# Kernel tuning notes

Hardware: AMD Instinct MI355X
Metric: run time of the kernel (lower is better)

Reference implementation:

```python
import jax, jax.numpy as jnp
import numpy as np

Hh, Ww, Cc = 8, 8, 16        # observation grid h, w, channels
N = Hh * Ww                  # 64 graph nodes (one per grid cell)
B = 4096                     # batch
HEADS, COUT = 4, 32          # GAT heads, per-head output dim (concat -> 128)
HID, ADIM = 128, 6           # hidden_dim, action_dim
GAT_OUT = N * HEADS * COUT   # 8192 flattened GAT output per sample
NEG = -9e15


def _grid_adj():
    # 4-connected grid graph with self loops (make_graph's static edge structure)
    A = np.zeros((N, N), np.int32)
    for r in range(Hh):
        for c in range(Ww):
            i = r * Ww + c
            A[i, i] = 1
            for dr, dc in ((1, 0), (-1, 0), (0, 1), (0, -1)):
                rr, cc = r + dr, c + dc
                if 0 <= rr < Hh and 0 <= cc < Ww:
                    A[i, rr * Ww + cc] = 1
    return jnp.asarray(A)


def setup_inputs() -> dict:
    key = jax.random.key(0)
    ks = iter(jax.random.split(key, 40))
    p = lambda *s: jax.random.normal(next(ks), s, jnp.float32) * 0.1
    z = lambda *s: jnp.zeros(s, jnp.float32)
    return dict(
        x=jax.random.normal(next(ks), (B, Hh * Ww * Cc), jnp.float32),
        adj=_grid_adj(),
        actor_h=z(B, HID), actor_c=z(B, HID),
        critic_h=z(B, HID), critic_c=z(B, HID),
        gat1_W=p(Cc, HEADS * COUT), gat1_b=z(HEADS * COUT), gat1_a=p(HEADS, 2 * COUT),
        d1_W=p(GAT_OUT, HID), d1_b=z(HID),
        lstm1_Wi=p(HID, 4 * HID), lstm1_Wh=p(HID, 4 * HID), lstm1_b=z(4 * HID),
        ln1_s=jnp.ones((HID,), jnp.float32), ln1_bi=z(HID),
        d2_W=p(HID, HID), d2_b=z(HID),
        d3_W=p(HID, HID), d3_b=z(HID),
        dout_W=p(HID, ADIM), dout_b=z(ADIM),
        gat2_W=p(Cc, HEADS * COUT), gat2_b=z(HEADS * COUT), gat2_a=p(HEADS, 2 * COUT),
        c1_W=p(GAT_OUT, HID), c1_b=z(HID),
        lstm2_Wi=p(HID, 4 * HID), lstm2_Wh=p(HID, 4 * HID), lstm2_b=z(4 * HID),
        ln2_s=jnp.ones((HID,), jnp.float32), ln2_bi=z(HID),
        c2_W=p(HID, HID), c2_b=z(HID),
        c3_W=p(HID, HID), c3_b=z(HID),
        cout_W=p(HID, 1), cout_b=z(1),
    )


def _gat(feats, adj, W, b, a):
    # feats: [B,N,Cc]; adj: [N,N] int; multi-head GAT with concat heads
    h = (feats @ W + b).reshape(B, N, HEADS, COUT)           # [B,N,H,C]
    ls = jnp.einsum('bnhc,hc->bnh', h, a[:, :COUT])          # source logit
    ld = jnp.einsum('bnhc,hc->bnh', h, a[:, COUT:])          # dest logit
    logits = jax.nn.leaky_relu(ls[:, :, None, :] + ld[:, None, :, :], 0.2)  # [B,N,N,H]
    logits = jnp.where(adj[None, :, :, None] > 0, logits, NEG)
    attn = jax.nn.softmax(logits, axis=2)                    # over neighbors
    return jnp.einsum('bnmh,bmhc->bnhc', attn, h).reshape(B, -1)  # [B, N*H*C]


def _lstm(h, c, xin, Wi, Wh, bh):
    # flax OptimizedLSTMCell: gates in order i,f,g,o; bias only on hidden path
    z = xin @ Wi + h @ Wh + bh
    i, f, g, o = jnp.split(z, 4, axis=-1)
    nc = jax.nn.sigmoid(f) * c + jax.nn.sigmoid(i) * jnp.tanh(g)
    nh = jax.nn.sigmoid(o) * jnp.tanh(nc)
    return nh, nc


def _ln(v, s, b):
    mu = v.mean(-1, keepdims=True)
    var = v.var(-1, keepdims=True)
    return (v - mu) * jax.lax.rsqrt(var + 1e-6) * s + b


def reference(x, adj, actor_h, actor_c, critic_h, critic_c,
              gat1_W, gat1_b, gat1_a, d1_W, d1_b,
              lstm1_Wi, lstm1_Wh, lstm1_b, ln1_s, ln1_bi,
              d2_W, d2_b, d3_W, d3_b, dout_W, dout_b,
              gat2_W, gat2_b, gat2_a, c1_W, c1_b,
              lstm2_Wi, lstm2_Wh, lstm2_b, ln2_s, ln2_bi,
              c2_W, c2_b, c3_W, c3_b, cout_W, cout_b):
    act = jnp.tanh
    feats = x.reshape(B, N, Cc)
    # actor branch
    am = act(_gat(feats, adj, gat1_W, gat1_b, gat1_a) @ d1_W + d1_b)
    a_h, a_c = _lstm(actor_h, actor_c, am, lstm1_Wi, lstm1_Wh, lstm1_b)
    am = _ln(a_h, ln1_s, ln1_bi)
    am = act(am @ d2_W + d2_b)
    am = act(am @ d3_W + d3_b)
    logits = am @ dout_W + dout_b                            # Categorical logits
    # critic branch
    cm = act(_gat(feats, adj, gat2_W, gat2_b, gat2_a) @ c1_W + c1_b)
    c_h, c_c = _lstm(critic_h, critic_c, cm, lstm2_Wi, lstm2_Wh, lstm2_b)
    cm = _ln(c_h, ln2_s, ln2_bi)
    cm = act(cm @ c2_W + c2_b)
    cm = act(cm @ c3_W + c3_b)
    value = (cm @ cout_W + cout_b).squeeze(-1)
    return logits, value, a_h, a_c, c_h, c_c
```

## Files before the change

kernel.cpp:

```cpp
#include <hip/hip_runtime.h>
#include <hip/hip_bf16.h>

#define BATCH 4096
#define NN    64
#define CIN   16
#define NHEAD 4
#define CO    32
#define HC    128
#define HID   128
#define ADIM  6
#define K1    8192
#define LDH   136
#define KSPLIT 8

typedef __attribute__((ext_vector_type(8))) short bf16x8;
typedef __attribute__((ext_vector_type(8))) unsigned short u16x8;
typedef __attribute__((ext_vector_type(4))) float f32x4;

__device__ __forceinline__ float bf2f(unsigned short u) {
    unsigned int v = ((unsigned int)u) << 16;
    return __uint_as_float(v);
}
__device__ __forceinline__ unsigned short f2bf(float x) {
    union { __hip_bfloat16 h; unsigned short u; } cv;
    cv.h = __float2bfloat16(x);
    return cv.u;
}
__device__ __forceinline__ float sigmf(float x) { return 1.f / (1.f + expf(-x)); }

__device__ __forceinline__ void gload_lds16(const void* g, void* l) {
    __builtin_amdgcn_global_load_lds(
        (const __attribute__((address_space(1))) unsigned int*)(uintptr_t)g,
        (__attribute__((address_space(3))) unsigned int*)(uintptr_t)l,
        16, 0, 0);
}

struct TJob { const float* in; unsigned short* out; int K; int N; int ldo; };
struct TJobs { TJob j[8]; };

__global__ __launch_bounds__(256) void k_prep(
    const float* __restrict__ d1W, const float* __restrict__ c1W,
    unsigned short* __restrict__ Wt1, unsigned short* __restrict__ Wt2,
    TJobs jobs,
    const float* __restrict__ ha, const float* __restrict__ hc,
    unsigned short* __restrict__ X,
    const int* __restrict__ adj, unsigned long long* __restrict__ masks,
    const float* __restrict__ l1b, const float* __restrict__ l2b,
    const float* __restrict__ b2,  const float* __restrict__ c2b,
    const float* __restrict__ b3,  const float* __restrict__ c3b,
    float* __restrict__ biasz, float* __restrict__ b2p, float* __restrict__ b3p,
    const float* __restrict__ g1W, const float* __restrict__ g2W,
    unsigned short* __restrict__ wtg)
{
    const int bid = blockIdx.x;
    const int t   = threadIdx.x;

    if (bid < 1024) {
        __shared__ float s[64][33];
        const int  zsel = bid >> 9;
        const float* W  = zsel ? c1W : d1W;
        unsigned short* Wt = zsel ? Wt2 : Wt1;
        const int k0 = (bid & 127) * 64;
        const int n0 = ((bid >> 7) & 3) * 32;
        const int kr = t >> 5, nc = t & 31;
#pragma unroll
        for (int i = 0; i < 8; ++i)
            s[kr + 8 * i][nc] = W[(size_t)(k0 + kr + 8 * i) * HC + n0 + nc];
        __syncthreads();
#pragma unroll
        for (int j = 0; j < 8; ++j) {
            const int idx = j * 256 + t;
            const int n = idx >> 6, k = idx & 63;
            Wt[(size_t)(n0 + n) * K1 + k0 + k] = f2bf(s[k][n]);
        }
    } else if (bid < 1536) {
        const int b   = bid - 1024;
        const int job = b >> 6, idx = b & 63;
        const TJob jb = jobs.j[job];
        const int ntk = jb.K >> 5, ntn = jb.N >> 5;
        if (idx >= ntk * ntn) return;
        const int tk = idx % ntk, tn = idx / ntk;
        __shared__ float s2[32][33];
        const int kr = t >> 5, nc = t & 31;
        const int k0 = tk * 32, n0 = tn * 32;
#pragma unroll
        for (int i = 0; i < 4; ++i)
            s2[kr + 8 * i][nc] = jb.in[(size_t)(k0 + kr + 8 * i) * jb.N + n0 + nc];
        __syncthreads();
#pragma unroll
        for (int i = 0; i < 4; ++i) {
            const int idx2 = i * 256 + t;
            const int n = idx2 >> 5, k = idx2 & 31;
            jb.out[(size_t)(n0 + n) * jb.ldo + k0 + k] = f2bf(s2[k][n]);
        }
    } else if (bid < 2560) {
        const int gid = (bid - 1536) * 256 + t;
        const int zi  = gid >> 17;
        const int rem = gid & 131071;
        const int s3  = rem >> 5, c4 = rem & 31;
        const float4 v = reinterpret_cast<const float4*>(zi ? hc : ha)[(size_t)s3 * 32 + c4];
        ushort4 u;
        u.x = f2bf(v.x); u.y = f2bf(v.y); u.z = f2bf(v.z); u.w = f2bf(v.w);
        reinterpret_cast<ushort4*>(X + (size_t)zi * BATCH * 256 + (size_t)s3 * 256 + 128)[c4] = u;
    } else {
#pragma unroll
        for (int it = 0; it < 4; ++it) {
            const int tt = t + it * 256;
            if (tt < NN) {
                unsigned long long m = 0ull;
                for (int j = 0; j < NN; ++j)
                    if (adj[tt * NN + j] > 0) m |= (1ull << j);
                masks[tt] = m;
            }
            biasz[tt] = (tt < 512) ? l1b[tt] : l2b[tt - 512];
            if (tt < HID) {
                b2p[tt]       = b2[tt];
                b2p[HID + tt] = c2b[tt];
                b3p[tt]       = b3[tt];
                b3p[HID + tt] = c3b[tt];
            }
        }
#pragma unroll
        for (int q = 0; q < 16; ++q) {
            const int idx = t * 16 + q;
            const int set = idx >> 11;
            const int rem = idx & 2047;
            const int col = rem >> 4, k = rem & 15;
            wtg[set * 2048 + col * 16 + k] = f2bf((set ? g2W : g1W)[k * HC + col]);
        }
    }
}

struct GatW { const unsigned short* Wt; const float* b; const float* a; unsigned short* out; };
struct GatArgs { GatW g[2]; };

__global__ __launch_bounds__(256) void k_gat(
    const float* __restrict__ x,
    const unsigned long long* __restrict__ masks,
    GatArgs ga, int zbase)
{
    const GatW gw = ga.g[zbase + blockIdx.y];
    const unsigned short* __restrict__ Wtg = gw.Wt;
    const float* __restrict__ bias = gw.b;
    const float* __restrict__ a    = gw.a;
    unsigned short* __restrict__ out = gw.out;

    union UBuf {
        struct { unsigned short feat[64][16]; unsigned short wt[128][16]; } stg;
        struct { float ls[64][4]; float ld[64][4]; } ph;
    };
    __shared__ UBuf u;
    __shared__ unsigned short s_h[64][LDH];
    __shared__ float s_bias[HC];
    __shared__ float s_a[4][68];
    __shared__ unsigned long long s_mask[NN];

    const int t = threadIdx.x;
    const int b = blockIdx.x;

    {
        const int n = t >> 2, c0 = (t & 3) * 4;
        const float4 v = reinterpret_cast<const float4*>(x + (size_t)b * (NN * CIN))[t];
        ushort4 q;
        q.x = f2bf(v.x); q.y = f2bf(v.y); q.z = f2bf(v.z); q.w = f2bf(v.w);
        *reinterpret_cast<ushort4*>(&u.stg.feat[n][c0]) = q;

        const int col = t >> 1, half = t & 1;
        const u16x8 wv = *reinterpret_cast<const u16x8*>(Wtg + col * 16 + half * 8);
        *reinterpret_cast<u16x8*>(&u.stg.wt[col][half * 8]) = wv;

        s_a[t >> 6][t & 63] = a[t];
        if (t < HC) s_bias[t] = bias[t];
        if (t < NN) s_mask[t] = masks[t];
    }
    __syncthreads();

    {
        const int w = t >> 6, lane = t & 63;
        const int row16 = lane & 15;
        const bool lo = lane < 32;
        const int k0 = (lane >> 4) * 8;
        const bf16x8 zf = { 0, 0, 0, 0, 0, 0, 0, 0 };
        bf16x8 aF, bF[8];
        aF = lo ? *reinterpret_cast<const bf16x8*>(&u.stg.feat[w * 16 + row16][k0]) : zf;
#pragma unroll
        for (int ct = 0; ct < 8; ++ct)
            bF[ct] = lo ? *reinterpret_cast<const bf16x8*>(&u.stg.wt[ct * 16 + row16][k0]) : zf;
        f32x4 acc[8] = {};
#pragma unroll
        for (int ct = 0; ct < 8; ++ct)
            acc[ct] = __builtin_amdgcn_mfma_f32_16x16x32_bf16(aF, bF[ct], acc[ct], 0, 0, 0);
#pragma unroll
        for (int ct = 0; ct < 8; ++ct) {
            const int col = ct * 16 + row16;
            const float bv = s_bias[col];
#pragma unroll
            for (int j = 0; j < 4; ++j)
                s_h[w * 16 + (lane >> 4) * 4 + j][col] = f2bf(acc[ct][j] + bv);
        }
    }
    __syncthreads();

    const int n  = t >> 2;
    const int hd = t & 3;

    {
        float ls = 0.f, ld = 0.f;
#pragma unroll
        for (int cb = 0; cb < 4; ++cb) {
            const u16x8 hv = *reinterpret_cast<const u16x8*>(&s_h[n][hd * 32 + cb * 8]);
            const float4 a1 = *reinterpret_cast<const float4*>(&s_a[hd][cb * 8]);
            const float4 a1b = *reinterpret_cast<const float4*>(&s_a[hd][cb * 8 + 4]);
            const float4 a2 = *reinterpret_cast<const float4*>(&s_a[hd][32 + cb * 8]);
            const float4 a2b = *reinterpret_cast<const float4*>(&s_a[hd][32 + cb * 8 + 4]);
            ls = fmaf(bf2f(hv[0]), a1.x, ls);  ls = fmaf(bf2f(hv[1]), a1.y, ls);
            ls = fmaf(bf2f(hv[2]), a1.z, ls);  ls = fmaf(bf2f(hv[3]), a1.w, ls);
            ls = fmaf(bf2f(hv[4]), a1b.x, ls); ls = fmaf(bf2f(hv[5]), a1b.y, ls);
            ls = fmaf(bf2f(hv[6]), a1b.z, ls); ls = fmaf(bf2f(hv[7]), a1b.w, ls);
            ld = fmaf(bf2f(hv[0]), a2.x, ld);  ld = fmaf(bf2f(hv[1]), a2.y, ld);
            ld = fmaf(bf2f(hv[2]), a2.z, ld);  ld = fmaf(bf2f(hv[3]), a2.w, ld);
            ld = fmaf(bf2f(hv[4]), a2b.x, ld); ld = fmaf(bf2f(hv[5]), a2b.y, ld);
            ld = fmaf(bf2f(hv[6]), a2b.z, ld); ld = fmaf(bf2f(hv[7]), a2b.w, ld);
        }
        u.ph.ls[n][hd] = ls;
        u.ph.ld[n][hd] = ld;
    }
    __syncthreads();

    {
        const unsigned long long m = s_mask[n];
        const int cand[5] = { n - 8, n - 1, n, n + 1, n + 8 };
        int  mc[5];
        bool ok[5];
#pragma unroll
        for (int e = 0; e < 5; ++e) {
            const int cm = cand[e];
            const bool inr = (cm >= 0) && (cm < NN);
            mc[e] = inr ? cm : n;
            ok[e] = inr && ((m >> mc[e]) & 1ull);
        }
        const float lsn = u.ph.ls[n][hd];
        float p[5];
        float sum = 0.f;
#pragma unroll
        for (int e = 0; e < 5; ++e) {
            float v = lsn + u.ph.ld[mc[e]][hd];
            v = (v > 0.f) ? v : 0.2f * v;
            p[e] = ok[e] ? __expf(v) : 0.f;
            sum += p[e];
        }
        const float inv = 1.f / sum;
#pragma unroll
        for (int e = 0; e < 5; ++e) p[e] *= inv;

        unsigned short* op = out + (size_t)b * K1 + n * HC + hd * CO;
#pragma unroll
        for (int cb = 0; cb < 4; ++cb) {
            float acc8[8] = {};
#pragma unroll
            for (int e = 0; e < 5; ++e) {
                const float pe = p[e];
                const u16x8 hv = *reinterpret_cast<const u16x8*>(
                    &s_h[mc[e]][hd * 32 + cb * 8]);
#pragma unroll
                for (int q = 0; q < 8; ++q)
                    acc8[q] = fmaf(pe, bf2f(hv[q]), acc8[q]);
            }
            u16x8 uo;
#pragma unroll
            for (int q = 0; q < 8; ++q) uo[q] = f2bf(acc8[q]);
            *reinterpret_cast<u16x8*>(op + cb * 8) = uo;
        }
    }
}

__global__ __launch_bounds__(256) void k_mmsk(
    const unsigned short* __restrict__ A0, const unsigned short* __restrict__ A1,
    const unsigned short* __restrict__ Bt0, const unsigned short* __restrict__ Bt1,
    float* __restrict__ accum)
{
    __shared__ unsigned short sbuf[2][160 * 64];

    const int br   = blockIdx.y;
    const unsigned short* A  = br ? A1 : A0;
    const unsigned short* Bt = br ? Bt1 : Bt0;
    float* acc_out = accum + (size_t)br * BATCH * HID;

    const int t    = threadIdx.x;
    const int w    = t >> 6;
    const int lane = t & 63;
    const int m0   = blockIdx.x * 32;
    const int kbase = blockIdx.z * (K1 / KSPLIT);
    const int kiters = (K1 / KSPLIT) / 64;

    const char* srcp[5];
    int ldsoff[5];
#pragma unroll
    for (int q = 0; q < 5; ++q) {
        const int c     = w * 5 + q;
        const int p     = c * 1024 + lane * 16;
        const int prow  = p >> 7;
        const int pslot = (p >> 4) & 7;
        const int lslot = pslot ^ (prow & 7);
        ldsoff[q] = c * 1024;
        if (c < 4)
            srcp[q] = (const char*)(A + (size_t)(m0 + prow) * K1 + kbase + lslot * 8);
        else
            srcp[q] = (const char*)(Bt + (size_t)(prow - 32) * K1 + kbase + lslot * 8);
    }

    f32x4 acc[2][2] = {};

#pragma unroll
    for (int q = 0; q < 5; ++q)
        gload_lds16(srcp[q], (char*)&sbuf[0][0] + ldsoff[q]);
    __syncthreads();

    int buf = 0;
    for (int it = 0; it < kiters; ++it) {
        if (it + 1 < kiters) {
            const size_t kbyte = (size_t)(it + 1) * 128;
#pragma unroll
            for (int q = 0; q < 5; ++q)
                gload_lds16(srcp[q] + kbyte, (char*)&sbuf[buf ^ 1][0] + ldsoff[q]);
        }
        const char* bb = (const char*)&sbuf[buf][0];
        bf16x8 aF[2][2], bF[2][2];
#pragma unroll
        for (int kb = 0; kb < 2; ++kb) {
            const int slot = kb * 4 + (lane >> 4);
#pragma unroll
            for (int rb = 0; rb < 2; ++rb) {
                const int row = rb * 16 + (lane & 15);
                aF[rb][kb] = *(const bf16x8*)(bb + row * 128 + ((slot ^ (row & 7)) << 4));
            }
#pragma unroll
            for (int cb = 0; cb < 2; ++cb) {
                const int row = 32 + w * 32 + cb * 16 + (lane & 15);
                bF[cb][kb] = *(const bf16x8*)(bb + row * 128 + ((slot ^ (row & 7)) << 4));
            }
        }
#pragma unroll
        for (int kb = 0; kb < 2; ++kb)
#pragma unroll
            for (int rb = 0; rb < 2; ++rb)
#pragma unroll
                for (int cb = 0; cb < 2; ++cb)
                    acc[rb][cb] = __builtin_amdgcn_mfma_f32_16x16x32_bf16(
                        aF[rb][kb], bF[cb][kb], acc[rb][cb], 0, 0, 0);
        __syncthreads();
        buf ^= 1;
    }

    const int col0 = w * 32;
    const int r0   = (lane >> 4) * 4;
    const int cc   = lane & 15;
#pragma unroll
    for (int rb = 0; rb < 2; ++rb)
#pragma unroll
        for (int cb = 0; cb < 2; ++cb) {
            const int col = col0 + cb * 16 + cc;
#pragma unroll
            for (int j = 0; j < 4; ++j) {
                const int row = m0 + rb * 16 + r0 + j;
                atomicAdd(&acc_out[(size_t)row * HID + col], acc[rb][cb][j]);
            }
        }
}

__global__ __launch_bounds__(256) void k_epi(
    const float* __restrict__ accum, const float* __restrict__ bias,
    unsigned short* __restrict__ Xo)
{
    const int gid = blockIdx.x * 256 + threadIdx.x;
    const int s = gid >> 5, c4 = gid & 31;
    const float4 v  = reinterpret_cast<const float4*>(accum)[gid];
    const float4 bv = reinterpret_cast<const float4*>(bias)[c4];
    ushort4 u;
    u.x = f2bf(tanhf(v.x + bv.x));
    u.y = f2bf(tanhf(v.y + bv.y));
    u.z = f2bf(tanhf(v.z + bv.z));
    u.w = f2bf(tanhf(v.w + bv.w));
    reinterpret_cast<ushort4*>(Xo + (size_t)s * 256)[c4] = u;
}

__global__ __launch_bounds__(256) void k_mm(
    const unsigned short* __restrict__ A, size_t aZ, int lda,
    const unsigned short* __restrict__ Bt, size_t bZ,
    const float* __restrict__ bias, size_t biasZ,
    float* __restrict__ outF, unsigned short* __restrict__ outB,
    size_t oZ, int ldo, int kiters, int act)
{
    __shared__ unsigned short sbuf[2][160 * 64];

    const int t    = threadIdx.x;
    const int w    = t >> 6;
    const int lane = t & 63;
    const int m0   = blockIdx.x * 32;
    const int n0   = blockIdx.y * 128;
    const int z    = blockIdx.z;
    const int K    = kiters * 64;

    const unsigned short* Az = A  + (size_t)z * aZ;
    const unsigned short* Bz = Bt + (size_t)z * bZ + (size_t)n0 * K;

    const char* srcp[5];
    int ldsoff[5];
#pragma unroll
    for (int q = 0; q < 5; ++q) {
        const int c     = w * 5 + q;
        const int p     = c * 1024 + lane * 16;
        const int prow  = p >> 7;
        const int pslot = (p >> 4) & 7;
        const int lslot = pslot ^ (prow & 7);
        ldsoff[q] = c * 1024;
        if (c < 4)
            srcp[q] = (const char*)(Az + (size_t)(m0 + prow) * lda + lslot * 8);
        else
            srcp[q] = (const char*)(Bz + (size_t)(prow - 32) * K + lslot * 8);
    }

    f32x4 acc[2][2] = {};

#pragma unroll
    for (int q = 0; q < 5; ++q)
        gload_lds16(srcp[q], (char*)&sbuf[0][0] + ldsoff[q]);
    __syncthreads();

    int buf = 0;
    for (int it = 0; it < kiters; ++it) {
        if (it + 1 < kiters) {
            const size_t kbyte = (size_t)(it + 1) * 128;
#pragma unroll
            for (int q = 0; q < 5; ++q)
                gload_lds16(srcp[q] + kbyte, (char*)&sbuf[buf ^ 1][0] + ldsoff[q]);
        }
        const char* bb = (const char*)&sbuf[buf][0];
        bf16x8 aF[2][2], bF[2][2];
#pragma unroll
        for (int kb = 0; kb < 2; ++kb) {
            const int slot = kb * 4 + (lane >> 4);
#pragma unroll
            for (int rb = 0; rb < 2; ++rb) {
                const int row = rb * 16 + (lane & 15);
                aF[rb][kb] = *(const bf16x8*)(bb + row * 128 + ((slot ^ (row & 7)) << 4));
            }
#pragma unroll
            for (int cb = 0; cb < 2; ++cb) {
                const int row = 32 + w * 32 + cb * 16 + (lane & 15);
                bF[cb][kb] = *(const bf16x8*)(bb + row * 128 + ((slot ^ (row & 7)) << 4));
            }
        }
#pragma unroll
        for (int kb = 0; kb < 2; ++kb)
#pragma unroll
            for (int rb = 0; rb < 2; ++rb)
#pragma unroll
                for (int cb = 0; cb < 2; ++cb)
                    acc[rb][cb] = __builtin_amdgcn_mfma_f32_16x16x32_bf16(
                        aF[rb][kb], bF[cb][kb], acc[rb][cb], 0, 0, 0);
        __syncthreads();
        buf ^= 1;
    }

    const int col0 = w * 32;
    const int r0   = (lane >> 4) * 4;
    const int cc   = lane & 15;
#pragma unroll
    for (int rb = 0; rb < 2; ++rb)
#pragma unroll
        for (int cb = 0; cb < 2; ++cb) {
            const int col = col0 + cb * 16 + cc;
            const float bv = bias ? bias[(size_t)z * biasZ + n0 + col] : 0.f;
#pragma unroll
            for (int j = 0; j < 4; ++j) {
                const int row = m0 + rb * 16 + r0 + j;
                float v = acc[rb][cb][j] + bv;
                if (act) v = tanhf(v);
                const size_t off = (size_t)z * oZ + (size_t)row * ldo + n0 + col;
                if (outB) outB[off] = f2bf(v);
                else      outF[off] = v;
            }
        }
}

__global__ __launch_bounds__(256) void k_tail(
    const float* __restrict__ zbuf,
    const float* __restrict__ c0a, const float* __restrict__ c0c,
    const float* __restrict__ sA,  const float* __restrict__ bA,
    const float* __restrict__ sC,  const float* __restrict__ bC,
    const unsigned short* __restrict__ W23t,
    const float* __restrict__ b2p, const float* __restrict__ b3p,
    const float* __restrict__ doW, const float* __restrict__ dob,
    const float* __restrict__ coW, const float* __restrict__ cob,
    float* __restrict__ hA, float* __restrict__ cA,
    float* __restrict__ hC, float* __restrict__ cC,
    float* __restrict__ logits, float* __restrict__ value)
{
    __shared__ unsigned short s_ln[32][LDH];
    __shared__ unsigned short s_t2[32][LDH];
    __shared__ unsigned short s_t3[32][LDH];
    __shared__ unsigned short s_w[128][LDH];

    const int t  = threadIdx.x;
    const int zi = blockIdx.y;
    const int s0 = blockIdx.x * 32;

    const unsigned short* W2 = W23t + (size_t)zi * HID * HID;
    const unsigned short* W3 = W23t + (size_t)(2 + zi) * HID * HID;

    {
        const int s  = t >> 3, l8 = t & 7;
        const int gb = s0 + s;
        const float* zr  = zbuf + (size_t)zi * BATCH * 512 + (size_t)gb * 512;
        const float* c0  = (zi ? c0c : c0a) + (size_t)gb * HID;
        float* oh = (zi ? hC : hA) + (size_t)gb * HID;
        float* oc = (zi ? cC : cA) + (size_t)gb * HID;
        const float* lns = zi ? sC : sA;
        const float* lnb = zi ? bC : bA;
        const int u0 = l8 * 16;

        float nh16[16];
        float sum = 0.f, sumsq = 0.f;
#pragma unroll
        for (int r4 = 0; r4 < 4; ++r4) {
            const int u = u0 + r4 * 4;
            const float4 gi = *reinterpret_cast<const float4*>(&zr[u]);
            const float4 gf = *reinterpret_cast<const float4*>(&zr[128 + u]);
            const float4 gg = *reinterpret_cast<const float4*>(&zr[256 + u]);
            const float4 go = *reinterpret_cast<const float4*>(&zr[384 + u]);
            const float4 cv = *reinterpret_cast<const float4*>(&c0[u]);
            float4 ncv, nhv;
            ncv.x = sigmf(gf.x) * cv.x + sigmf(gi.x) * tanhf(gg.x);
            ncv.y = sigmf(gf.y) * cv.y + sigmf(gi.y) * tanhf(gg.y);
            ncv.z = sigmf(gf.z) * cv.z + sigmf(gi.z) * tanhf(gg.z);
            ncv.w = sigmf(gf.w) * cv.w + sigmf(gi.w) * tanhf(gg.w);
            nhv.x = sigmf(go.x) * tanhf(ncv.x);
            nhv.y = sigmf(go.y) * tanhf(ncv.y);
            nhv.z = sigmf(go.z) * tanhf(ncv.z);
            nhv.w = sigmf(go.w) * tanhf(ncv.w);
            *reinterpret_cast<float4*>(&oc[u]) = ncv;
            *reinterpret_cast<float4*>(&oh[u]) = nhv;
            nh16[r4 * 4 + 0] = nhv.x; nh16[r4 * 4 + 1] = nhv.y;
            nh16[r4 * 4 + 2] = nhv.z; nh16[r4 * 4 + 3] = nhv.w;
            sum   += nhv.x + nhv.y + nhv.z + nhv.w;
            sumsq += nhv.x * nhv.x + nhv.y * nhv.y + nhv.z * nhv.z + nhv.w * nhv.w;
        }
        for (int msk = 1; msk < 8; msk <<= 1) {
            sum   += __shfl_xor(sum, msk, 8);
            sumsq += __shfl_xor(sumsq, msk, 8);
        }
        const float mu   = sum * (1.f / 128.f);
        const float var  = sumsq * (1.f / 128.f) - mu * mu;
        const float rstd = rsqrtf(var + 1e-6f);
        u16x8 lo, hi;
#pragma unroll
        for (int r = 0; r < 8; ++r) {
            lo[r] = f2bf((nh16[r] - mu) * rstd * lns[u0 + r] + lnb[u0 + r]);
            hi[r] = f2bf((nh16[8 + r] - mu) * rstd * lns[u0 + 8 + r] + lnb[u0 + 8 + r]);
        }
        *reinterpret_cast<u16x8*>(&s_ln[s][u0])     = lo;
        *reinterpret_cast<u16x8*>(&s_ln[s][u0 + 8]) = hi;

        const int col = t >> 1, half = (t & 1) * 64;
#pragma unroll
        for (int q = 0; q < 8; ++q) {
            const u16x8 wv = *reinterpret_cast<const u16x8*>(W2 + col * HID + half + q * 8);
            *reinterpret_cast<u16x8*>(&s_w[col][half + q * 8]) = wv;
        }
    }
    __syncthreads();

    const int w = t >> 6, lane = t & 63;
    const int row16 = lane & 15, k08 = (lane >> 4) * 8;

    {
        f32x4 acc[2][2] = {};
#pragma unroll
        for (int ks = 0; ks < 4; ++ks) {
            bf16x8 aF[2], bF[2];
#pragma unroll
            for (int rt = 0; rt < 2; ++rt)
                aF[rt] = *reinterpret_cast<const bf16x8*>(&s_ln[rt * 16 + row16][ks * 32 + k08]);
#pragma unroll
            for (int ct = 0; ct < 2; ++ct)
                bF[ct] = *reinterpret_cast<const bf16x8*>(&s_w[w * 32 + ct * 16 + row16][ks * 32 + k08]);
#pragma unroll
            for (int rt = 0; rt < 2; ++rt)
#pragma unroll
                for (int ct = 0; ct < 2; ++ct)
                    acc[rt][ct] = __builtin_amdgcn_mfma_f32_16x16x32_bf16(
                        aF[rt], bF[ct], acc[rt][ct], 0, 0, 0);
        }
#pragma unroll
        for (int rt = 0; rt < 2; ++rt)
#pragma unroll
            for (int ct = 0; ct < 2; ++ct) {
                const int col = w * 32 + ct * 16 + row16;
                const float bv = b2p[zi * HID + col];
#pragma unroll
                for (int j = 0; j < 4; ++j)
                    s_t2[rt * 16 + (lane >> 4) * 4 + j][col] = f2bf(tanhf(acc[rt][ct][j] + bv));
            }
    }
    __syncthreads();

    {
        const int col = t >> 1, half = (t & 1) * 64;
#pragma unroll
        for (int q = 0; q < 8; ++q) {
            const u16x8 wv = *reinterpret_cast<const u16x8*>(W3 + col * HID + half + q * 8);
            *reinterpret_cast<u16x8*>(&s_w[col][half + q * 8]) = wv;
        }
    }
    __syncthreads();

    {
        f32x4 acc[2][2] = {};
#pragma unroll
        for (int ks = 0; ks < 4; ++ks) {
            bf16x8 aF[2], bF[2];
#pragma unroll
            for (int rt = 0; rt < 2; ++rt)
                aF[rt] = *reinterpret_cast<const bf16x8*>(&s_t2[rt * 16 + row16][ks * 32 + k08]);
#pragma unroll
            for (int ct = 0; ct < 2; ++ct)
                bF[ct] = *reinterpret_cast<const bf16x8*>(&s_w[w * 32 + ct * 16 + row16][ks * 32 + k08]);
#pragma unroll
            for (int rt = 0; rt < 2; ++rt)
#pragma unroll
                for (int ct = 0; ct < 2; ++ct)
                    acc[rt][ct] = __builtin_amdgcn_mfma_f32_16x16x32_bf16(
                        aF[rt], bF[ct], acc[rt][ct], 0, 0, 0);
        }
#pragma unroll
        for (int rt = 0; rt < 2; ++rt)
#pragma unroll
            for (int ct = 0; ct < 2; ++ct) {
                const int col = w * 32 + ct * 16 + row16;
                const float bv = b3p[zi * HID + col];
#pragma unroll
                for (int j = 0; j < 4; ++j)
                    s_t3[rt * 16 + (lane >> 4) * 4 + j][col] = f2bf(tanhf(acc[rt][ct][j] + bv));
            }
    }
    __syncthreads();

    if (zi == 0) {
        if (t < 32 * ADIM) {
            const int s = t / ADIM, a2 = t % ADIM;
            float acc = dob[a2];
            for (int k = 0; k < HID; ++k)
                acc = fmaf(bf2f(s_t3[s][k]), doW[k * ADIM + a2], acc);
            logits[(size_t)(s0 + s) * ADIM + a2] = acc;
        }
    } else {
        if (t < 32) {
            float acc = cob[0];
            for (int k = 0; k < HID; ++k)
                acc = fmaf(bf2f(s_t3[t][k]), coW[k], acc);
            value[s0 + t] = acc;
        }
    }
}

extern "C" void kernel_launch(void* const* d_in, const int* in_sizes, int n_in,
                              void* d_out, int out_size, void* d_ws, size_t ws_size,
                              hipStream_t stream)
{
    (void)in_sizes; (void)n_in; (void)out_size;

    const float* x        = (const float*)d_in[0];
    const int*   adj      = (const int*)  d_in[1];
    const float* actor_h  = (const float*)d_in[2];
    const float* actor_c  = (const float*)d_in[3];
    const float* critic_h = (const float*)d_in[4];
    const float* critic_c = (const float*)d_in[5];
    const float* gat1_W   = (const float*)d_in[6];
    const float* gat1_b   = (const float*)d_in[7];
    const float* gat1_a   = (const float*)d_in[8];
    const float* d1_W     = (const float*)d_in[9];
    const float* d1_b     = (const float*)d_in[10];
    const float* l1_Wi    = (const float*)d_in[11];
    const float* l1_Wh    = (const float*)d_in[12];
    const float* l1_b     = (const float*)d_in[13];
    const float* ln1_s    = (const float*)d_in[14];
    const float* ln1_b    = (const float*)d_in[15];
    const float* d2_W     = (const float*)d_in[16];
    const float* d2_b     = (const float*)d_in[17];
    const float* d3_W     = (const float*)d_in[18];
    const float* d3_b     = (const float*)d_in[19];
    const float* dout_W   = (const float*)d_in[20];
    const float* dout_b   = (const float*)d_in[21];
    const float* gat2_W   = (const float*)d_in[22];
    const float* gat2_b   = (const float*)d_in[23];
    const float* gat2_a   = (const float*)d_in[24];
    const float* c1_W     = (const float*)d_in[25];
    const float* c1_b     = (const float*)d_in[26];
    const float* l2_Wi    = (const float*)d_in[27];
    const float* l2_Wh    = (const float*)d_in[28];
    const float* l2_b     = (const float*)d_in[29];
    const float* ln2_s    = (const float*)d_in[30];
    const float* ln2_b    = (const float*)d_in[31];
    const float* c2_W     = (const float*)d_in[32];
    const float* c2_b     = (const float*)d_in[33];
    const float* c3_W     = (const float*)d_in[34];
    const float* c3_b     = (const float*)d_in[35];
    const float* cout_W   = (const float*)d_in[36];
    const float* cout_b   = (const float*)d_in[37];

    float* out      = (float*)d_out;
    float* o_logits = out;
    float* o_value  = out + (size_t)BATCH * ADIM;
    float* o_ah     = o_value + BATCH;
    float* o_ac     = o_ah + (size_t)BATCH * HID;
    float* o_ch     = o_ac + (size_t)BATCH * HID;
    float* o_cc     = o_ch + (size_t)BATCH * HID;

    char* ws = (char*)d_ws;
    const size_t MB = 1024 * 1024;
    const size_t KB = 1024;
    unsigned long long* masks = (unsigned long long*)ws;
    float* bias_z = (float*)(ws + 4 * KB);
    float* b2p    = (float*)(ws + 8 * KB);
    float* b3p    = (float*)(ws + 12 * KB);
    unsigned short* wtg = (unsigned short*)(ws + 16 * KB);
    float* accum  = (float*)(ws + 64 * KB);
    unsigned short* Wt1  = (unsigned short*)(ws + 64 * KB + 4 * MB);
    unsigned short* Wt2  = (unsigned short*)(ws + 64 * KB + 6 * MB);
    unsigned short* Wcat = (unsigned short*)(ws + 64 * KB + 8 * MB);
    unsigned short* W23t = (unsigned short*)(ws + 64 * KB + 8 * MB + 512 * KB);
    unsigned short* X    = (unsigned short*)(ws + 64 * KB + 8 * MB + 768 * KB);
    const size_t off_big = 64 * KB + 8 * MB + 768 * KB + 4 * MB;
    char* big = ws + off_big;
    unsigned short* gatA = (unsigned short*)big;
    const bool dual = ws_size >= off_big + 128 * MB;
    unsigned short* gatB = dual ? (unsigned short*)(big + 64 * MB) : gatA;
    float*          zbuf = (float*)big;

    TJobs tj;
    tj.j[0] = { l1_Wi, Wcat,                        HID, 512, 256 };
    tj.j[1] = { l1_Wh, Wcat + 128,                  HID, 512, 256 };
    tj.j[2] = { l2_Wi, Wcat + 512 * 256,            HID, 512, 256 };
    tj.j[3] = { l2_Wh, Wcat + 512 * 256 + 128,      HID, 512, 256 };
    tj.j[4] = { d2_W,  W23t,                        HID, HID, HID };
    tj.j[5] = { c2_W,  W23t + 128 * 128,            HID, HID, HID };
    tj.j[6] = { d3_W,  W23t + 2 * 128 * 128,        HID, HID, HID };
    tj.j[7] = { c3_W,  W23t + 3 * 128 * 128,        HID, HID, HID };
    hipLaunchKernelGGL(k_prep, dim3(2561), dim3(256), 0, stream,
                       d1_W, c1_W, Wt1, Wt2, tj,
                       actor_h, critic_h, X,
                       adj, masks, l1_b, l2_b, d2_b, c2_b, d3_b, c3_b,
                       bias_z, b2p, b3p, gat1_W, gat2_W, wtg);

    GatArgs ga;
    ga.g[0] = { wtg,        gat1_b, gat1_a, gatA };
    ga.g[1] = { wtg + 2048, gat2_b, gat2_a, gatB };

    if (dual) {
        hipMemsetAsync(accum, 0, (size_t)2 * BATCH * HID * 4, stream);
        hipLaunchKernelGGL(k_gat, dim3(BATCH, 2), dim3(256), 0, stream,
                           x, masks, ga, 0);
        hipLaunchKernelGGL(k_mmsk, dim3(BATCH / 32, 2, KSPLIT), dim3(256), 0, stream,
                           gatA, gatB, Wt1, Wt2, accum);
        hipLaunchKernelGGL(k_epi, dim3(512), dim3(256), 0, stream,
                           accum, d1_b, X);
        hipLaunchKernelGGL(k_epi, dim3(512), dim3(256), 0, stream,
                           accum + (size_t)BATCH * HID, c1_b, X + (size_t)BATCH * 256);
    } else {
        hipLaunchKernelGGL(k_gat, dim3(BATCH, 1), dim3(256), 0, stream,
                           x, masks, ga, 0);
        hipMemsetAsync(accum, 0, (size_t)BATCH * HID * 4, stream);
        hipLaunchKernelGGL(k_mmsk, dim3(BATCH / 32, 1, KSPLIT), dim3(256), 0, stream,
                           gatA, gatA, Wt1, Wt1, accum);
        hipLaunchKernelGGL(k_epi, dim3(512), dim3(256), 0, stream,
                           accum, d1_b, X);
        hipLaunchKernelGGL(k_gat, dim3(BATCH, 1), dim3(256), 0, stream,
                           x, masks, ga, 1);
        hipMemsetAsync(accum, 0, (size_t)BATCH * HID * 4, stream);
        hipLaunchKernelGGL(k_mmsk, dim3(BATCH / 32, 1, KSPLIT), dim3(256), 0, stream,
                           gatA, gatA, Wt2, Wt2, accum);
        hipLaunchKernelGGL(k_epi, dim3(512), dim3(256), 0, stream,
                           accum, c1_b, X + (size_t)BATCH * 256);
    }

    hipLaunchKernelGGL(k_mm, dim3(BATCH / 32, 4, 2), dim3(256), 0, stream,
                       X, (size_t)BATCH * 256, 256, Wcat, (size_t)512 * 256,
                       bias_z, (size_t)512,
                       zbuf, (unsigned short*)nullptr, (size_t)BATCH * 512, 512, 4, 0);

    hipLaunchKernelGGL(k_tail, dim3(BATCH / 32, 2), dim3(256), 0, stream,
                       zbuf, actor_c, critic_c, ln1_s, ln1_b, ln2_s, ln2_b,
                       W23t, b2p, b3p, dout_W, dout_b, cout_W, cout_b,
                       o_ah, o_ac, o_ch, o_cc, o_logits, o_value);
}
```

Before: 144.6 us.

## Fold GAT attention vectors into weights and aggregate neighbours via MFMA

Precomputes W·a and b·a in the prep kernel so the per-node source and destination attention scores come out of an extra MFMA column tile, instead of a scalar dot-product phase and its barrier. Neighbour aggregation is recast as a dense bf16 matmul of a 64x64 attention matrix P (mostly zeros) with the transposed head features, done on MFMA in two passes. This replaces the scalar FMA loops with matrix-core work but adds shared memory (s_hT, s_P), zero-filling, extra barriers, and scalar 2-byte global stores for the output. Rounding attention weights and W·a to bf16 also changes precision.

```diff
diff --git a/kernel.cpp b/kernel.cpp
--- a/kernel.cpp
+++ b/kernel.cpp
@@ -50,7 +50,10 @@
     const float* __restrict__ b3,  const float* __restrict__ c3b,
     float* __restrict__ biasz, float* __restrict__ b2p, float* __restrict__ b3p,
     const float* __restrict__ g1W, const float* __restrict__ g2W,
-    unsigned short* __restrict__ wtg)
+    const float* __restrict__ g1a, const float* __restrict__ g2a,
+    const float* __restrict__ g1b, const float* __restrict__ g2b,
+    unsigned short* __restrict__ wtg,
+    float* __restrict__ blsld)
 {
     const int bid = blockIdx.x;
     const int t   = threadIdx.x;
@@ -126,12 +129,34 @@
             const int set = idx >> 11;
             const int rem = idx & 2047;
             const int col = rem >> 4, k = rem & 15;
-            wtg[set * 2048 + col * 16 + k] = f2bf((set ? g2W : g1W)[k * HC + col]);
-        }
-    }
-}
-
-struct GatW { const unsigned short* Wt; const float* b; const float* a; unsigned short* out; };
+            wtg[set * 2304 + col * 16 + k] = f2bf((set ? g2W : g1W)[k * HC + col]);
+        }
+        {
+            const int set = t >> 7, rem = t & 127;
+            const int e = rem >> 4, k = rem & 15;
+            const float* W  = set ? g2W : g1W;
+            const float* aa = set ? g2a : g1a;
+            const int hdh = e & 3, off = (e < 4) ? 0 : 32;
+            float v = 0.f;
+            for (int c = 0; c < 32; ++c)
+                v += W[k * HC + hdh * 32 + c] * aa[hdh * 64 + off + c];
+            wtg[set * 2304 + (128 + e) * 16 + k] = f2bf(v);
+            wtg[set * 2304 + (136 + e) * 16 + k] = 0;
+        }
+        if (t < 16) {
+            const int s2 = t >> 3, e2 = t & 7;
+            const float* bb2 = s2 ? g2b : g1b;
+            const float* aa2 = s2 ? g2a : g1a;
+            const int h2 = e2 & 3, o2 = (e2 < 4) ? 0 : 32;
+            float bv = 0.f;
+            for (int c = 0; c < 32; ++c)
+                bv += bb2[h2 * 32 + c] * aa2[h2 * 64 + o2 + c];
+            blsld[s2 * 8 + e2] = bv;
+        }
+    }
+}
+
+struct GatW { const unsigned short* Wt; const float* b; const float* bls; unsigned short* out; };
 struct GatArgs { GatW g[2]; };
 
 __global__ __launch_bounds__(256) void k_gat(
@@ -142,17 +167,17 @@
     const GatW gw = ga.g[zbase + blockIdx.y];
     const unsigned short* __restrict__ Wtg = gw.Wt;
     const float* __restrict__ bias = gw.b;
-    const float* __restrict__ a    = gw.a;
+    const float* __restrict__ bls  = gw.bls;
     unsigned short* __restrict__ out = gw.out;
 
-    union UBuf {
-        struct { unsigned short feat[64][16]; unsigned short wt[128][16]; } stg;
-        struct { float ls[64][4]; float ld[64][4]; } ph;
-    };
-    __shared__ UBuf u;
-    __shared__ unsigned short s_h[64][LDH];
+    __shared__ unsigned short s_feat[64][16];
+    __shared__ unsigned short s_wt[144][16];
+    __shared__ unsigned short s_hT[128][72];
+    __shared__ unsigned short s_P[2][64][72];
+    __shared__ float s_ls[64][4];
+    __shared__ float s_ld[64][4];
     __shared__ float s_bias[HC];
-    __shared__ float s_a[4][68];
+    __shared__ float s_bls[8];
     __shared__ unsigned long long s_mask[NN];
 
     const int t = threadIdx.x;
@@ -163,75 +188,63 @@
         const float4 v = reinterpret_cast<const float4*>(x + (size_t)b * (NN * CIN))[t];
         ushort4 q;
         q.x = f2bf(v.x); q.y = f2bf(v.y); q.z = f2bf(v.z); q.w = f2bf(v.w);
-        *reinterpret_cast<ushort4*>(&u.stg.feat[n][c0]) = q;
-
-        const int col = t >> 1, half = t & 1;
-        const u16x8 wv = *reinterpret_cast<const u16x8*>(Wtg + col * 16 + half * 8);
-        *reinterpret_cast<u16x8*>(&u.stg.wt[col][half * 8]) = wv;
-
-        s_a[t >> 6][t & 63] = a[t];
+        *reinterpret_cast<ushort4*>(&s_feat[n][c0]) = q;
+        if (t < 144) {
+            *reinterpret_cast<u16x8*>(&s_wt[t][0]) = *reinterpret_cast<const u16x8*>(Wtg + t * 16);
+            *reinterpret_cast<u16x8*>(&s_wt[t][8]) = *reinterpret_cast<const u16x8*>(Wtg + t * 16 + 8);
+        }
         if (t < HC) s_bias[t] = bias[t];
+        if (t < 8)  s_bls[t] = bls[t];
         if (t < NN) s_mask[t] = masks[t];
     }
     __syncthreads();
 
+    const int w = t >> 6, lane = t & 63;
+    const int row16 = lane & 15;
+    const int jr4   = lane >> 4;
+
     {
-        const int w = t >> 6, lane = t & 63;
-        const int row16 = lane & 15;
         const bool lo = lane < 32;
-        const int k0 = (lane >> 4) * 8;
+        const int k0 = (jr4 & 1) * 8;
         const bf16x8 zf = { 0, 0, 0, 0, 0, 0, 0, 0 };
-        bf16x8 aF, bF[8];
-        aF = lo ? *reinterpret_cast<const bf16x8*>(&u.stg.feat[w * 16 + row16][k0]) : zf;
-#pragma unroll
-        for (int ct = 0; ct < 8; ++ct)
-            bF[ct] = lo ? *reinterpret_cast<const bf16x8*>(&u.stg.wt[ct * 16 + row16][k0]) : zf;
-        f32x4 acc[8] = {};
-#pragma unroll
-        for (int ct = 0; ct < 8; ++ct)
+        const bf16x8 aF = lo ? *reinterpret_cast<const bf16x8*>(&s_feat[w * 16 + row16][k0]) : zf;
+        bf16x8 bF[9];
+#pragma unroll
+        for (int ct = 0; ct < 9; ++ct)
+            bF[ct] = lo ? *reinterpret_cast<const bf16x8*>(&s_wt[ct * 16 + row16][k0]) : zf;
+        f32x4 acc[9] = {};
+#pragma unroll
+        for (int ct = 0; ct < 9; ++ct)
             acc[ct] = __builtin_amdgcn_mfma_f32_16x16x32_bf16(aF, bF[ct], acc[ct], 0, 0, 0);
 #pragma unroll
         for (int ct = 0; ct < 8; ++ct) {
             const int col = ct * 16 + row16;
             const float bv = s_bias[col];
-#pragma unroll
-            for (int j = 0; j < 4; ++j)
-                s_h[w * 16 + (lane >> 4) * 4 + j][col] = f2bf(acc[ct][j] + bv);
+            ushort4 q;
+            q.x = f2bf(acc[ct][0] + bv);
+            q.y = f2bf(acc[ct][1] + bv);
+            q.z = f2bf(acc[ct][2] + bv);
+            q.w = f2bf(acc[ct][3] + bv);
+            *reinterpret_cast<ushort4*>(&s_hT[col][w * 16 + jr4 * 4]) = q;
+        }
+        if (row16 < 8) {
+            const float bb = s_bls[row16];
+#pragma unroll
+            for (int j = 0; j < 4; ++j) {
+                const int r = w * 16 + jr4 * 4 + j;
+                if (row16 < 4) s_ls[r][row16]     = acc[8][j] + bb;
+                else           s_ld[r][row16 - 4] = acc[8][j] + bb;
+            }
         }
     }
     __syncthreads();
 
     const int n  = t >> 2;
     const int hd = t & 3;
-
-    {
-        float ls = 0.f, ld = 0.f;
-#pragma unroll
-        for (int cb = 0; cb < 4; ++cb) {
-            const u16x8 hv = *reinterpret_cast<const u16x8*>(&s_h[n][hd * 32 + cb * 8]);
-            const float4 a1 = *reinterpret_cast<const float4*>(&s_a[hd][cb * 8]);
-            const float4 a1b = *reinterpret_cast<const float4*>(&s_a[hd][cb * 8 + 4]);
-            const float4 a2 = *reinterpret_cast<const float4*>(&s_a[hd][32 + cb * 8]);
-            const float4 a2b = *reinterpret_cast<const float4*>(&s_a[hd][32 + cb * 8 + 4]);
-            ls = fmaf(bf2f(hv[0]), a1.x, ls);  ls = fmaf(bf2f(hv[1]), a1.y, ls);
-            ls = fmaf(bf2f(hv[2]), a1.z, ls);  ls = fmaf(bf2f(hv[3]), a1.w, ls);
-            ls = fmaf(bf2f(hv[4]), a1b.x, ls); ls = fmaf(bf2f(hv[5]), a1b.y, ls);
-            ls = fmaf(bf2f(hv[6]), a1b.z, ls); ls = fmaf(bf2f(hv[7]), a1b.w, ls);
-            ld = fmaf(bf2f(hv[0]), a2.x, ld);  ld = fmaf(bf2f(hv[1]), a2.y, ld);
-            ld = fmaf(bf2f(hv[2]), a2.z, ld);  ld = fmaf(bf2f(hv[3]), a2.w, ld);
-            ld = fmaf(bf2f(hv[4]), a2b.x, ld); ld = fmaf(bf2f(hv[5]), a2b.y, ld);
-            ld = fmaf(bf2f(hv[6]), a2b.z, ld); ld = fmaf(bf2f(hv[7]), a2b.w, ld);
-        }
-        u.ph.ls[n][hd] = ls;
-        u.ph.ld[n][hd] = ld;
-    }
-    __syncthreads();
-
+    float p[5]; int mc[5]; bool ok[5];
     {
         const unsigned long long m = s_mask[n];
         const int cand[5] = { n - 8, n - 1, n, n + 1, n + 8 };
-        int  mc[5];
-        bool ok[5];
 #pragma unroll
         for (int e = 0; e < 5; ++e) {
             const int cm = cand[e];
@@ -239,12 +252,11 @@
             mc[e] = inr ? cm : n;
             ok[e] = inr && ((m >> mc[e]) & 1ull);
         }
-        const float lsn = u.ph.ls[n][hd];
-        float p[5];
+        const float lsn = s_ls[n][hd];
         float sum = 0.f;
 #pragma unroll
         for (int e = 0; e < 5; ++e) {
-            float v = lsn + u.ph.ld[mc[e]][hd];
+            float v = lsn + s_ld[mc[e]][hd];
             v = (v > 0.f) ? v : 0.2f * v;
             p[e] = ok[e] ? __expf(v) : 0.f;
             sum += p[e];
@@ -252,25 +264,60 @@
         const float inv = 1.f / sum;
 #pragma unroll
         for (int e = 0; e < 5; ++e) p[e] *= inv;
-
-        unsigned short* op = out + (size_t)b * K1 + n * HC + hd * CO;
-#pragma unroll
-        for (int cb = 0; cb < 4; ++cb) {
-            float acc8[8] = {};
-#pragma unroll
-            for (int e = 0; e < 5; ++e) {
-                const float pe = p[e];
-                const u16x8 hv = *reinterpret_cast<const u16x8*>(
-                    &s_h[mc[e]][hd * 32 + cb * 8]);
-#pragma unroll
-                for (int q = 0; q < 8; ++q)
-                    acc8[q] = fmaf(pe, bf2f(hv[q]), acc8[q]);
-            }
-            u16x8 uo;
-#pragma unroll
-            for (int q = 0; q < 8; ++q) uo[q] = f2bf(acc8[q]);
-            *reinterpret_cast<u16x8*>(op + cb * 8) = uo;
-        }
+    }
+
+    {
+        char* pb = (char*)&s_P[0][0][0];
+#pragma unroll
+        for (int i = 0; i < 9; ++i)
+            *reinterpret_cast<unsigned long long*>(pb + t * 72 + i * 8) = 0ull;
+    }
+    __syncthreads();
+
+    unsigned short* ob = out + (size_t)b * K1;
+
+#pragma unroll
+    for (int pass = 0; pass < 2; ++pass) {
+        if ((hd >> 1) == pass) {
+#pragma unroll
+            for (int e = 0; e < 5; ++e)
+                if (ok[e]) s_P[hd & 1][n][mc[e]] = f2bf(p[e]);
+        }
+        __syncthreads();
+
+        const int hh  = pass * 2 + (w >> 1);
+        const int ph  = w >> 1;
+        const int mtb = (w & 1) * 2;
+        f32x4 acc[2][2] = {};
+#pragma unroll
+        for (int kt = 0; kt < 2; ++kt) {
+            const int kof = kt * 32 + jr4 * 8;
+            bf16x8 aF[2], bF[2];
+#pragma unroll
+            for (int mtl = 0; mtl < 2; ++mtl)
+                aF[mtl] = *reinterpret_cast<const bf16x8*>(&s_P[ph][(mtb + mtl) * 16 + row16][kof]);
+#pragma unroll
+            for (int nt = 0; nt < 2; ++nt)
+                bF[nt] = *reinterpret_cast<const bf16x8*>(&s_hT[hh * 32 + nt * 16 + row16][kof]);
+#pragma unroll
+            for (int mtl = 0; mtl < 2; ++mtl)
+#pragma unroll
+                for (int nt = 0; nt < 2; ++nt)
+                    acc[mtl][nt] = __builtin_amdgcn_mfma_f32_16x16x32_bf16(
+                        aF[mtl], bF[nt], acc[mtl][nt], 0, 0, 0);
+        }
+#pragma unroll
+        for (int mtl = 0; mtl < 2; ++mtl)
+#pragma unroll
+            for (int nt = 0; nt < 2; ++nt) {
+                const int ch = hh * 32 + nt * 16 + row16;
+#pragma unroll
+                for (int j = 0; j < 4; ++j) {
+                    const int node = (mtb + mtl) * 16 + jr4 * 4 + j;
+                    ob[node * HC + ch] = f2bf(acc[mtl][nt][j]);
+                }
+            }
+        if (pass == 0) __syncthreads();
     }
 }
 
@@ -725,6 +772,7 @@
     float* b2p    = (float*)(ws + 8 * KB);
     float* b3p    = (float*)(ws + 12 * KB);
     unsigned short* wtg = (unsigned short*)(ws + 16 * KB);
+    float* blsld  = (float*)(ws + 60 * KB);
     float* accum  = (float*)(ws + 64 * KB);
     unsigned short* Wt1  = (unsigned short*)(ws + 64 * KB + 4 * MB);
     unsigned short* Wt2  = (unsigned short*)(ws + 64 * KB + 6 * MB);
@@ -751,11 +799,12 @@
                        d1_W, c1_W, Wt1, Wt2, tj,
                        actor_h, critic_h, X,
                        adj, masks, l1_b, l2_b, d2_b, c2_b, d3_b, c3_b,
-                       bias_z, b2p, b3p, gat1_W, gat2_W, wtg);
+                       bias_z, b2p, b3p, gat1_W, gat2_W,
+                       gat1_a, gat2_a, gat1_b, gat2_b, wtg, blsld);
 
     GatArgs ga;
-    ga.g[0] = { wtg,        gat1_b, gat1_a, gatA };
-    ga.g[1] = { wtg + 2048, gat2_b, gat2_a, gatB };
+    ga.g[0] = { wtg,        gat1_b, blsld,     gatA };
+    ga.g[1] = { wtg + 2304, gat2_b, blsld + 8, gatB };
 
     if (dual) {
         hipMemsetAsync(accum, 0, (size_t)2 * BATCH * HID * 4, stream);
```

After: 142.7 us. No clear change (-1.3%).
